# Optimization experiments

Measured on AMD Instinct MI355X. Metric: run time of the kernel, lower is better.

## Reference

```python
import math
import jax, jax.numpy as jnp
import numpy as np

B, L, H, D = 1, 2048, 16, 64
M = 24            # nb_features
WINDOW = 128      # local_context / window_size
SCALE = 0.125     # softmax_scale = 1/sqrt(D)
MASK_VAL = -10000.0
EPS = 1e-4        # SBPerformerFeatures eps


def setup_inputs() -> dict:
    key = jax.random.key(0)
    k1, k2 = jax.random.split(key)
    qkv = jax.random.normal(k1, (B, L, 3, H, D), dtype=jnp.float32)
    proj = jax.random.normal(k2, (M, D), dtype=jnp.float32)  # Performer random features
    return {"qkv": qkv, "proj": proj}


def _performer_features(x, proj, is_query):
    # Softmax-kernel random features with separate log scale (scatterbrain SBPerformerFeatures).
    # exp(t*q.k) ~= exp(q_log + k_log) * <q_prime, k_prime>
    dn = math.sqrt(SCALE)
    xs = x * dn                                            # (b,h,l,d)
    x_dash = jnp.einsum('bhld,md->bhlm', xs, proj)         # (b,h,l,m)
    x_norm = 0.5 * jnp.sum(xs * xs, axis=-1, keepdims=True)
    half_log_m = 0.5 * math.log(M)
    if is_query:
        stab = jax.lax.stop_gradient(jnp.max(x_dash, axis=-1, keepdims=True))
        prime = jnp.exp(x_dash - stab) + EPS               # per-row stabilized
        log_scale = stab - x_norm - half_log_m             # (b,h,l,1)
    else:
        stab = jax.lax.stop_gradient(jnp.max(x_dash, axis=(-1, -2), keepdims=True))
        prime = jnp.exp(x_dash - x_norm - stab) + EPS      # norm folded in (needed for cumsum)
        log_scale = stab - half_log_m                      # (b,h,1,1)
    return prime, log_scale


def _band_mask(n):
    idx = jnp.arange(n)
    diff = idx[:, None] - idx[None, :]                     # i - j
    return jnp.where((diff >= 0) & (diff <= WINDOW), 0.0, MASK_VAL)  # (L,L)


def _forward(qkv, proj):
    q, k, v = qkv[:, :, 0], qkv[:, :, 1], qkv[:, :, 2]     # (b,l,h,d)
    q = jnp.transpose(q, (0, 2, 1, 3))                     # (b,h,l,d)
    k = jnp.transpose(k, (0, 2, 1, 3))
    v = jnp.transpose(v, (0, 2, 1, 3))

    # --- GlobalPerformer path ---
    q_prime, q_log = _performer_features(q, proj, True)    # (b,h,l,m), (b,h,l,1)
    k_prime, k_log = _performer_features(k, proj, False)   # (b,h,l,m), (b,h,1,1)
    global_scale = q_log + k_log                           # (b,h,l,1)

    k_cum = jnp.cumsum(k_prime, axis=2)
    global_out_cumsum = jnp.einsum('bhlm,bhlm->bhl', q_prime, k_cum)
    # causal_dot_product: out_i = q'_i . sum_{j<=i} k'_j v_j^T
    kv = jnp.cumsum(k_prime[..., :, None] * v[..., None, :], axis=2)   # (b,h,l,m,d)
    global_out = jnp.einsum('bhlm,bhlmd->bhld', q_prime, kv)

    mask = _band_mask(L)
    p_scores = jnp.einsum('bhme,bhne->bhmn', q_prime, k_prime) * SCALE
    global_qk = jnp.maximum(p_scores + mask[None, None], 0.0)  # masked_fill(<=0, 0)

    # --- Local exact softmax path ---
    scores = jnp.einsum('bhme,bhne->bhmn', q, k) * SCALE
    local_qk = scores + mask[None, None]
    qk_lse = jax.scipy.special.logsumexp(local_qk, axis=-1, keepdims=True)  # (b,h,l,1)

    gqk_sum = jnp.sum(global_qk, axis=-1, keepdims=True)
    global_log_norm = jnp.log(jnp.maximum(global_out_cumsum[..., None] - gqk_sum, 1e-24)) + global_scale
    log_norm = jnp.logaddexp(qk_lse, global_log_norm)      # (b,h,l,1)
    global_prime_scale = jnp.exp(global_scale - log_norm)  # (b,h,l,1)

    local_score = jax.nn.softmax(local_qk - log_norm, axis=-1) - global_qk * global_prime_scale
    out = jnp.einsum('bhmn,bhnd->bhmd', local_score, v) + global_out * global_prime_scale
    return jnp.transpose(out, (0, 2, 1, 3))                # (b,l,h,d)


def reference(qkv, proj):
    return _forward(qkv, proj)
```

## Files before the change

kernel.cpp:

```cpp
#include <hip/hip_runtime.h>
#include <hip/hip_bf16.h>

#define L_SEQ 2048
#define NH 16
#define DH 64
#define NM 24
#define NCH 32
#define SCALE_F 0.125f
#define EPS_F 1e-4f
#define DN_F 0.35355339059327373f
#define HLM_F 1.5890269151739727f

typedef __attribute__((ext_vector_type(8))) short short8v;
typedef __attribute__((ext_vector_type(4))) float f32x4;

__device__ __forceinline__ unsigned short f2bf(float x) {
  unsigned u = __float_as_uint(x);
  u += 0x7FFFu + ((u >> 16) & 1u);
  return (unsigned short)(u >> 16);
}
__device__ __forceinline__ unsigned pk2(float a, float b) {
  return (unsigned)f2bf(a) | ((unsigned)f2bf(b) << 16);
}
__device__ __forceinline__ float stab_from_pmax(const float* __restrict__ pmax, int h, int t) {
  float v = pmax[h * 32 + (t & 31)];
  v = fmaxf(v, __shfl_xor(v, 1));  v = fmaxf(v, __shfl_xor(v, 2));
  v = fmaxf(v, __shfl_xor(v, 4));  v = fmaxf(v, __shfl_xor(v, 8));
  v = fmaxf(v, __shfl_xor(v, 16));
  return v;
}

__global__ __launch_bounds__(256) void k1_feat(
    const float* __restrict__ qkv, const float* __restrict__ proj,
    float* __restrict__ kdash, float* __restrict__ knorm,
    float* __restrict__ qdash, float* __restrict__ qnorm,
    float* __restrict__ pmax, unsigned* __restrict__ kbw, unsigned* __restrict__ qbw)
{
  __shared__ __attribute__((aligned(16))) float sP[24][68];
  __shared__ __attribute__((aligned(16))) float sX[64][68];
  __shared__ float sRed[256];
  const int c = blockIdx.x, h = blockIdx.y, t = threadIdx.x;
  for (int i = t; i < 24 * 64; i += 256) sP[i >> 6][i & 63] = proj[i];
  float lmax = -1e30f;
  const int r = t >> 2, mg = t & 3;
  for (int qk = 0; qk < 2; ++qk) {
    const int slot = qk ? 0 : 1;
    __syncthreads();
    for (int i = t; i < 1024; i += 256) {
      int rr = i >> 4, d4 = (i & 15) * 4;
      int l = c * 64 + rr;
      *(float4*)&sX[rr][d4] = *(const float4*)(qkv + (((size_t)l * 3 + slot) * NH + h) * DH + d4);
    }
    __syncthreads();
    unsigned* dstw = qk ? qbw : kbw;
    for (int w = t; w < 2048; w += 256) {
      int rr = w >> 5, wo = w & 31;
      int l = c * 64 + rr;
      float2 xv = *(const float2*)&sX[rr][2 * wo];
      dstw[((size_t)h * L_SEQ + l) * 32 + (wo ^ ((rr & 7) << 2))] = pk2(xv.x, xv.y);
    }
    float acc[6] = {0.f, 0.f, 0.f, 0.f, 0.f, 0.f};
    float sq = 0.f;
    for (int d4 = 0; d4 < 16; ++d4) {
      float4 xv = *(const float4*)&sX[r][d4 * 4];
      sq += xv.x * xv.x; sq += xv.y * xv.y; sq += xv.z * xv.z; sq += xv.w * xv.w;
#pragma unroll
      for (int i = 0; i < 6; ++i) {
        float4 pv = *(const float4*)&sP[mg * 6 + i][d4 * 4];
        acc[i] += xv.x * pv.x; acc[i] += xv.y * pv.y;
        acc[i] += xv.z * pv.z; acc[i] += xv.w * pv.w;
      }
    }
    int l = c * 64 + r;
    float* dsh = qk ? qdash : kdash;
#pragma unroll
    for (int i = 0; i < 6; ++i) {
      float v = acc[i] * DN_F;
      dsh[((size_t)h * L_SEQ + l) * 24 + mg * 6 + i] = v;
      if (!qk) lmax = fmaxf(lmax, v);
    }
    if (mg == 0) (qk ? qnorm : knorm)[h * L_SEQ + l] = 0.5f * SCALE_F * sq;
  }
  sRed[t] = lmax;
  __syncthreads();
#pragma unroll
  for (int s = 128; s > 0; s >>= 1) {
    if (t < s) sRed[t] = fmaxf(sRed[t], sRed[t + s]);
    __syncthreads();
  }
  if (t == 0) pmax[h * 32 + c] = sRed[0];
}

__global__ __launch_bounds__(256) void k3_kprime(
    const float* __restrict__ qkv, const float* __restrict__ kdash,
    const float* __restrict__ knorm, const float* __restrict__ pmax,
    unsigned* __restrict__ kpw, float* __restrict__ kpfx, float* __restrict__ kvs,
    unsigned* __restrict__ vtw)
{
  __shared__ float sKp[64][25];
  __shared__ __attribute__((aligned(16))) float sV[64][68];
  const int c = blockIdx.x, h = blockIdx.y, t = threadIdx.x;
  const float stab = stab_from_pmax(pmax, h, t);
  for (int i = t; i < 1024; i += 256) {
    int rr = i >> 4, d4 = (i & 15) * 4;
    int l = c * 64 + rr;
    *(float4*)&sV[rr][d4] = *(const float4*)(qkv + (((size_t)l * 3 + 2) * NH + h) * DH + d4);
  }
  for (int i = t; i < 1536; i += 256) {
    int r = i / 24, m = i % 24;
    int l = c * 64 + r;
    sKp[r][m] = __expf(kdash[((size_t)h * L_SEQ + l) * 24 + m] - knorm[h * L_SEQ + l] - stab) + EPS_F;
  }
  __syncthreads();
  for (int w = t; w < 1024; w += 256) {
    int r = w >> 4, wo = w & 15;
    int l = c * 64 + r;
    float a = (wo < 12) ? sKp[r][2 * wo] : 0.f;
    float bb = (wo < 12) ? sKp[r][2 * wo + 1] : 0.f;
    kpw[((size_t)h * L_SEQ + l) * 16 + (wo ^ ((r & 3) << 2))] = pk2(a, bb);
  }
  for (int w = t; w < 2048; w += 256) {
    int d = w >> 5, jp = w & 31;
    vtw[((size_t)h * NCH + c) * 2048 + d * 32 + (jp ^ ((d & 7) << 2))] = pk2(sV[2 * jp][d], sV[2 * jp + 1][d]);
  }
  if (t < 192) {
    const int m = t % 24, dO = (t / 24) * 8;
    float a0x = 0.f, a0y = 0.f, a0z = 0.f, a0w = 0.f;
    float a1x = 0.f, a1y = 0.f, a1z = 0.f, a1w = 0.f;
    for (int r2 = 0; r2 < 64; ++r2) {
      float kp = sKp[r2][m];
      float4 v0 = *(const float4*)&sV[r2][dO];
      float4 v1 = *(const float4*)&sV[r2][dO + 4];
      a0x += kp * v0.x; a0y += kp * v0.y; a0z += kp * v0.z; a0w += kp * v0.w;
      a1x += kp * v1.x; a1y += kp * v1.y; a1z += kp * v1.z; a1w += kp * v1.w;
    }
    float* dst = kvs + ((size_t)h * NCH + c) * 1536 + m * 64 + dO;
    float4 o0 = {a0x, a0y, a0z, a0w};
    float4 o1 = {a1x, a1y, a1z, a1w};
    *(float4*)dst = o0;
    *(float4*)(dst + 4) = o1;
  }
  if (t < 24) {
    float run = 0.f;
    for (int r2 = 0; r2 < 64; ++r2) {
      run += sKp[r2][t];
      kpfx[((size_t)h * L_SEQ + c * 64 + r2) * 24 + t] = run;
    }
  }
}

__global__ __launch_bounds__(256, 2) void k6_attn(
    const unsigned* __restrict__ kpw, const float* __restrict__ kpfx,
    const float* __restrict__ kvs, const unsigned* __restrict__ vtw,
    const float* __restrict__ qdash, const float* __restrict__ qnorm,
    const float* __restrict__ pmax, const unsigned* __restrict__ kbw,
    const unsigned* __restrict__ qbw, float* __restrict__ out)
{
  __shared__ __attribute__((aligned(16))) char lds[62304];
  char* sKW = lds;
  char* sKp = lds + 24576;
  char* sQV = lds + 36864;
  char* sQp = lds + 45056;
  float* sQpF = (float*)(lds + 49152);
  float* sSum = (float*)(lds + 55296);
  float* sGps = sSum + 64;
  float* sRin = sGps + 64;
  float* sKcx = (float*)(lds + 56064);
  float* sPfx = (float*)(lds + 56160);

  const int b = blockIdx.x, h = blockIdx.y, t = threadIdx.x;
  const int wv = t >> 6, lane = t & 63, g = lane >> 4, ln = lane & 15;
  const int keybase = b * 64 - 128;
  const int jmin = (b >= 2) ? 0 : (128 - 64 * b);
  const int rA = wv * 16 + ln;

  for (int w = t; w < 1536; w += 256) {
    int r = w >> 3, q4 = w & 7;
    int l = keybase + r; l = l < 0 ? 0 : l;
    *(uint4*)(sKW + r * 128 + q4 * 16) = *(const uint4*)(kbw + ((size_t)h * L_SEQ + l) * 32 + q4 * 4);
  }
  for (int w = t; w < 512; w += 256) {
    int r = w >> 3, q4 = w & 7;
    int l = b * 64 + r;
    *(uint4*)(sQV + r * 128 + q4 * 16) = *(const uint4*)(qbw + ((size_t)h * L_SEQ + l) * 32 + q4 * 4);
  }
  for (int w = t; w < 768; w += 256) {
    int r = w >> 2, q4 = w & 3;
    int l = keybase + r; l = l < 0 ? 0 : l;
    *(uint4*)(sKp + r * 64 + q4 * 16) = *(const uint4*)(kpw + ((size_t)h * L_SEQ + l) * 16 + q4 * 4);
  }
  const float stab = stab_from_pmax(pmax, h, t);
  {
    float accp[6] = {0.f, 0.f, 0.f, 0.f, 0.f, 0.f};
    for (int bp = 0; bp < b; ++bp) {
      const float* src = kvs + ((size_t)h * NCH + bp) * 1536;
#pragma unroll
      for (int j = 0; j < 6; ++j) accp[j] += src[t + j * 256];
    }
#pragma unroll
    for (int j = 0; j < 6; ++j) sPfx[t + j * 256] = accp[j];
  }
  if (t < 24) {
    float runk = 0.f;
    for (int bp = 0; bp < b; ++bp)
      runk += kpfx[((size_t)h * L_SEQ + bp * 64 + 63) * 24 + t];
    sKcx[t] = runk;
  }
  float qlog = 0.f;
  if (t < 64) {
    int r = t, l = b * 64 + r;
    const float* qdp = qdash + ((size_t)h * L_SEQ + l) * 24;
    float qd[24], mx = -1e30f;
#pragma unroll
    for (int m = 0; m < 24; ++m) { qd[m] = qdp[m]; mx = fmaxf(mx, qd[m]); }
    float qpv[24];
#pragma unroll
    for (int m = 0; m < 24; ++m) { qpv[m] = __expf(qd[m] - mx) + EPS_F; sQpF[r * 24 + m] = qpv[m]; }
    qlog = mx - qnorm[h * L_SEQ + l] - HLM_F;
#pragma unroll
    for (int wo = 0; wo < 16; ++wo) {
      float a = (wo < 12) ? qpv[2 * wo] : 0.f;
      float bb = (wo < 12) ? qpv[2 * wo + 1] : 0.f;
      *(unsigned*)(sQp + (r * 64 + (((wo * 4)) ^ ((r & 3) << 4)))) = pk2(a, bb);
    }
  }
  __syncthreads();

  float eF[12][4];
  float rs[4] = {0.f, 0.f, 0.f, 0.f};
  short8v aS0 = *(const short8v*)(sQV + (rA * 128 + ((g * 16) ^ ((rA & 7) << 4))));
  short8v aS1 = *(const short8v*)(sQV + (rA * 128 + ((64 + g * 16) ^ ((rA & 7) << 4))));
#pragma unroll
  for (int nt = 0; nt < 12; ++nt) {
    int rB = nt * 16 + ln;
    short8v b0 = *(const short8v*)(sKW + (rB * 128 + ((g * 16) ^ ((rB & 7) << 4))));
    short8v b1 = *(const short8v*)(sKW + (rB * 128 + ((64 + g * 16) ^ ((rB & 7) << 4))));
    f32x4 acc = {0.f, 0.f, 0.f, 0.f};
    acc = __builtin_amdgcn_mfma_f32_16x16x32_bf16(aS0, b0, acc, 0, 0, 0);
    acc = __builtin_amdgcn_mfma_f32_16x16x32_bf16(aS1, b1, acc, 0, 0, 0);
    int j = nt * 16 + ln;
#pragma unroll
    for (int reg = 0; reg < 4; ++reg) {
      int rl = wv * 16 + g * 4 + reg;
      float e = 0.f;
      if (j >= rl && j <= rl + 128 && j >= jmin) e = __expf(SCALE_F * acc[reg]);
      eF[nt][reg] = e;
      rs[reg] += e;
    }
  }
#pragma unroll
  for (int reg = 0; reg < 4; ++reg) {
    float v = rs[reg];
    v += __shfl_xor(v, 1); v += __shfl_xor(v, 2);
    v += __shfl_xor(v, 4); v += __shfl_xor(v, 8);
    if (ln == 0) sSum[wv * 16 + g * 4 + reg] = v;
  }

  float pF[12][4];
  short8v aP = *(const short8v*)(sQp + (rA * 64 + ((g * 16) ^ ((rA & 3) << 4))));
#pragma unroll
  for (int nt = 0; nt < 12; ++nt) {
    int rB = nt * 16 + ln;
    short8v bp = *(const short8v*)(sKp + (rB * 64 + ((g * 16) ^ ((rB & 3) << 4))));
    f32x4 acc = {0.f, 0.f, 0.f, 0.f};
    acc = __builtin_amdgcn_mfma_f32_16x16x32_bf16(aP, bp, acc, 0, 0, 0);
#pragma unroll
    for (int reg = 0; reg < 4; ++reg) pF[nt][reg] = acc[reg];
  }
  __syncthreads();

  if (t < 64) {
    int r = t, l = b * 64 + r;
    const float* kfc = kpfx + ((size_t)h * L_SEQ + l) * 24;
    int b1i = (b >= 1) ? b - 1 : 0;
    int b2i = (b >= 2) ? b - 2 : 0;
    int rm1 = (r >= 1) ? r - 1 : 0;
    const float* T1p = kpfx + ((size_t)h * L_SEQ + b1i * 64 + 63) * 24;
    const float* T2p = kpfx + ((size_t)h * L_SEQ + b2i * 64 + 63) * 24;
    const float* S2p = kpfx + ((size_t)h * L_SEQ + b2i * 64 + rm1) * 24;
    float f1 = (b >= 1) ? 1.f : 0.f;
    float f2 = (b >= 2) ? 1.f : 0.f;
    float fr = (b >= 2 && r >= 1) ? 1.f : 0.f;
    float psc = 0.f, kcs = 0.f, bnd = 0.f;
#pragma unroll
    for (int m = 0; m < 24; ++m) {
      float qp = sQpF[r * 24 + m];
      float kc = kfc[m];
      psc += qp * kc;
      kcs += qp * sKcx[m];
      bnd += qp * (kc + f1 * T1p[m] + f2 * T2p[m] - fr * S2p[m]);
    }
    float goc = kcs + psc;
    float gqk = SCALE_F * bnd;
    float se = sSum[r];
    float lse = __logf(se);
    float gscale = qlog + stab - HLM_F;
    float gln = __logf(fmaxf(goc - gqk, 1e-24f)) + gscale;
    float mx2 = fmaxf(lse, gln), mn2 = fminf(lse, gln);
    float lognorm = mx2 + log1pf(__expf(mn2 - mx2));
    sGps[r] = __expf(gscale - lognorm);
    sRin[r] = 1.f / se;
  }
  __syncthreads();

  float gpr[4], rin[4];
#pragma unroll
  for (int reg = 0; reg < 4; ++reg) {
    int rl = wv * 16 + g * 4 + reg;
    gpr[reg] = sGps[rl];
    rin[reg] = sRin[rl];
  }
#pragma unroll
  for (int nt = 0; nt < 12; ++nt) {
    int j = nt * 16 + ln;
#pragma unroll
    for (int reg = 0; reg < 4; ++reg) {
      int rl = wv * 16 + g * 4 + reg;
      bool causal = (j >= 128) && (j <= 128 + rl);
      bool bprev = (j >= rl) && (j < 128) && (j >= jmin);
      float coef = causal ? (1.f - SCALE_F) * gpr[reg] : (bprev ? -SCALE_F * gpr[reg] : 0.f);
      float wgt = eF[nt][reg] * rin[reg] + coef * pF[nt][reg];
      float wn = __shfl_xor(wgt, 1);
      if ((ln & 1) == 0) {
        *(unsigned*)(sKW + (rl * 384 + ((j * 2) ^ ((rl & 7) << 4)))) = pk2(wgt, wn);
      }
    }
  }
  __syncthreads();

  for (int w = t; w < 1024; w += 256) {
    int d = w >> 4, mp = w & 15;
    int m0 = 2 * mp, m1 = m0 + 1;
    float a = (m0 < 24) ? sPfx[m0 * 64 + d] : 0.f;
    float bb = (m1 < 24) ? sPfx[m1 * 64 + d] : 0.f;
    *(unsigned*)(sKp + (d * 64 + ((mp * 4) ^ ((d & 3) << 4)))) = pk2(a, bb);
  }

  f32x4 oF[4];
#pragma unroll
  for (int dt = 0; dt < 4; ++dt) { f32x4 z = {0.f, 0.f, 0.f, 0.f}; oF[dt] = z; }
  for (int vt3 = 0; vt3 < 3; ++vt3) {
    int lt = b - 2 + vt3; lt = lt < 0 ? 0 : lt;
    for (int w = t; w < 512; w += 256) {
      *(uint4*)(sQV + w * 16) = *(const uint4*)(vtw + ((size_t)h * NCH + lt) * 2048 + w * 4);
    }
    __syncthreads();
#pragma unroll
    for (int ks = 0; ks < 2; ++ks) {
      short8v aw = *(const short8v*)(sKW + (rA * 384 + ((vt3 * 128 + ks * 64 + g * 16) ^ ((rA & 7) << 4))));
#pragma unroll
      for (int dt = 0; dt < 4; ++dt) {
        int rB = dt * 16 + ln;
        short8v bv = *(const short8v*)(sQV + (rB * 128 + ((ks * 64 + g * 16) ^ ((rB & 7) << 4))));
        oF[dt] = __builtin_amdgcn_mfma_f32_16x16x32_bf16(aw, bv, oF[dt], 0, 0, 0);
      }
    }
    __syncthreads();
  }

  short8v aq = *(const short8v*)(sQp + (rA * 64 + ((g * 16) ^ ((rA & 3) << 4))));
  f32x4 ogF[4];
#pragma unroll
  for (int dt = 0; dt < 4; ++dt) {
    int rB = dt * 16 + ln;
    short8v bg = *(const short8v*)(sKp + (rB * 64 + ((g * 16) ^ ((rB & 3) << 4))));
    f32x4 z = {0.f, 0.f, 0.f, 0.f};
    ogF[dt] = __builtin_amdgcn_mfma_f32_16x16x32_bf16(aq, bg, z, 0, 0, 0);
  }

#pragma unroll
  for (int dt = 0; dt < 4; ++dt) {
    int d = dt * 16 + ln;
#pragma unroll
    for (int reg = 0; reg < 4; ++reg) {
      int rl = wv * 16 + g * 4 + reg;
      int l = b * 64 + rl;
      out[((size_t)l * NH + h) * DH + d] = oF[dt][reg] + gpr[reg] * ogF[dt][reg];
    }
  }
}

extern "C" void kernel_launch(void* const* d_in, const int* in_sizes, int n_in,
                              void* d_out, int out_size, void* d_ws, size_t ws_size,
                              hipStream_t stream)
{
  const float* qkv = (const float*)d_in[0];
  const float* proj = (const float*)d_in[1];
  float* out = (float*)d_out;
  char* ws = (char*)d_ws;

  float* kdash   = (float*)(ws + 0);
  float* qdash   = (float*)(ws + 3145728);
  float* knorm   = (float*)(ws + 6291456);
  float* qnorm   = (float*)(ws + 6422528);
  float* pmax    = (float*)(ws + 6553600);
  unsigned* kbw  = (unsigned*)(ws + 6555648);
  unsigned* qbw  = (unsigned*)(ws + 10749952);
  unsigned* kpw  = (unsigned*)(ws + 14944256);
  float* kpfx    = (float*)(ws + 17041408);
  unsigned* vtw  = (unsigned*)(ws + 20187136);
  float* kvs     = (float*)(ws + 24381440);

  k1_feat<<<dim3(32, 16), 256, 0, stream>>>(qkv, proj, kdash, knorm, qdash, qnorm, pmax, kbw, qbw);
  k3_kprime<<<dim3(32, 16), 256, 0, stream>>>(qkv, kdash, knorm, pmax, kpw, kpfx, kvs, vtw);
  k6_attn<<<dim3(32, 16), 256, 0, stream>>>(kpw, kpfx, kvs, vtw, qdash, qnorm, pmax, kbw, qbw, out);
}
```

Measured before the change: 125.7 us.

## Fuse three attention kernels into one cooperative kernel with grid syncs

Replaces the three-kernel pipeline (feature projection, key-prime/prefix, attention) with one cooperative kernel that uses two grid-wide syncs. Query features, bf16 tiles and V tiles stay in LDS across phases, so the qdash/qnorm/qbw workspace round trips and two launch gaps go away. The prefix-sum loop over kvs chunks is also unrolled by four to raise memory-level parallelism. The cost is grid.sync overhead and the constraint that all 512 blocks must be co-resident, which is why the launch asks for two blocks per CU and roughly 80KB of LDS each. If the cooperative launch fails, it falls back to the original three kernels.

```diff
diff --git a/kernel.cpp b/kernel.cpp
--- a/kernel.cpp
+++ b/kernel.cpp
@@ -1,10 +1,12 @@
 #include <hip/hip_runtime.h>
 #include <hip/hip_bf16.h>
+#include <hip/hip_cooperative_groups.h>
+
+namespace cg = cooperative_groups;
 
 #define L_SEQ 2048
 #define NH 16
 #define DH 64
-#define NM 24
 #define NCH 32
 #define SCALE_F 0.125f
 #define EPS_F 1e-4f
@@ -28,6 +30,396 @@
   v = fmaxf(v, __shfl_xor(v, 4));  v = fmaxf(v, __shfl_xor(v, 8));
   v = fmaxf(v, __shfl_xor(v, 16));
   return v;
+}
+
+#define LDS_BYTES 80512
+
+__global__ __launch_bounds__(256, 2) void fused_attn(
+    const float* __restrict__ qkv, const float* __restrict__ proj,
+    float* __restrict__ pmax, unsigned* __restrict__ kbw,
+    unsigned* __restrict__ kpw, float* __restrict__ kpfx,
+    float* __restrict__ kvs, unsigned* __restrict__ vtw,
+    float* __restrict__ out)
+{
+  __shared__ __align__(16) char lds[LDS_BYTES];
+  char* A  = lds;
+  char* B  = lds + 24576;
+  char* C  = lds + 36864;
+  char* D  = lds + 45056;
+  char* E  = lds + 53248;
+  char* F  = lds + 61440;
+  float* G = (float*)(lds + 65536);
+  float* H = (float*)(lds + 71680);
+  float* sRed  = (float*)(lds + 78336);
+  float* qlogA = (float*)(lds + 79360);
+  float* sKcx  = (float*)(lds + 79616);
+  float* sSum  = (float*)(lds + 79744);
+  float* sGps  = (float*)(lds + 80000);
+  float* sRin  = (float*)(lds + 80256);
+
+  const int b = blockIdx.x, h = blockIdx.y, t = threadIdx.x;
+  const int r4 = t >> 2, mg = t & 3;
+  cg::grid_group grid = cg::this_grid();
+
+  float* sP = (float*)D;
+  float* sX = (float*)A;
+  for (int i = t; i < 1536; i += 256) sP[(i >> 6) * 68 + (i & 63)] = proj[i];
+
+  float kd[6];
+  float sqk = 0.f;
+  float lmax = -1e30f;
+
+  for (int qk = 0; qk < 2; ++qk) {
+    const int slot = qk ? 0 : 1;
+    __syncthreads();
+    for (int i = t; i < 1024; i += 256) {
+      int rr = i >> 4, q = i & 15;
+      int l = b * 64 + rr;
+      *(float4*)&sX[rr * 64 + 4 * (q ^ (rr & 15))] =
+          *(const float4*)(qkv + (((size_t)l * 3 + slot) * NH + h) * DH + 4 * q);
+    }
+    __syncthreads();
+    for (int w = t; w < 2048; w += 256) {
+      int rr = w >> 5, wo = w & 31;
+      int q = wo >> 1, sub = (wo & 1) * 2;
+      const float* px = &sX[rr * 64 + 4 * (q ^ (rr & 15)) + sub];
+      unsigned word = pk2(px[0], px[1]);
+      int swo = wo ^ ((rr & 7) << 2);
+      if (qk == 0) {
+        kbw[((size_t)h * L_SEQ + b * 64 + rr) * 32 + swo] = word;
+        *(unsigned*)(A + 16384 + rr * 128 + 4 * swo) = word;
+      } else {
+        *(unsigned*)(C + rr * 128 + 4 * swo) = word;
+      }
+    }
+    float acc[6] = {0.f, 0.f, 0.f, 0.f, 0.f, 0.f};
+    float sq = 0.f;
+    for (int d4 = 0; d4 < 16; ++d4) {
+      float4 xv = *(const float4*)&sX[r4 * 64 + 4 * (d4 ^ (r4 & 15))];
+      sq += xv.x * xv.x; sq += xv.y * xv.y; sq += xv.z * xv.z; sq += xv.w * xv.w;
+#pragma unroll
+      for (int i = 0; i < 6; ++i) {
+        float4 pv = *(const float4*)&sP[(mg * 6 + i) * 68 + d4 * 4];
+        acc[i] += xv.x * pv.x; acc[i] += xv.y * pv.y;
+        acc[i] += xv.z * pv.z; acc[i] += xv.w * pv.w;
+      }
+    }
+    if (qk == 0) {
+#pragma unroll
+      for (int i = 0; i < 6; ++i) { kd[i] = acc[i] * DN_F; lmax = fmaxf(lmax, kd[i]); }
+      sqk = sq;
+    } else {
+      float qd6[6]; float mx = -1e30f;
+#pragma unroll
+      for (int i = 0; i < 6; ++i) { qd6[i] = acc[i] * DN_F; mx = fmaxf(mx, qd6[i]); }
+      mx = fmaxf(mx, __shfl_xor(mx, 1));
+      mx = fmaxf(mx, __shfl_xor(mx, 2));
+      float qpv[6];
+#pragma unroll
+      for (int i = 0; i < 6; ++i) {
+        qpv[i] = __expf(qd6[i] - mx) + EPS_F;
+        G[r4 * 24 + mg * 6 + i] = qpv[i];
+      }
+#pragma unroll
+      for (int j = 0; j < 3; ++j)
+        *(unsigned*)(F + r4 * 64 + 4 * ((3 * mg + j) ^ ((r4 & 3) << 2))) = pk2(qpv[2 * j], qpv[2 * j + 1]);
+      if (mg == 0) {
+#pragma unroll
+        for (int j = 0; j < 4; ++j)
+          *(unsigned*)(F + r4 * 64 + 4 * ((12 + j) ^ ((r4 & 3) << 2))) = 0u;
+        qlogA[r4] = mx - 0.5f * SCALE_F * sq - HLM_F;
+      }
+    }
+  }
+  sRed[t] = lmax;
+  __syncthreads();
+#pragma unroll
+  for (int s = 128; s > 0; s >>= 1) {
+    if (t < s) sRed[t] = fmaxf(sRed[t], sRed[t + s]);
+    __syncthreads();
+  }
+  if (t == 0) pmax[h * 32 + b] = sRed[0];
+
+  grid.sync();
+
+  const float stab = stab_from_pmax(pmax, h, t);
+  float* sV = (float*)A;
+  for (int i = t; i < 1024; i += 256) {
+    int rr = i >> 4, q = i & 15;
+    int l = b * 64 + rr;
+    *(float4*)&sV[rr * 64 + 4 * (q ^ (rr & 15))] =
+        *(const float4*)(qkv + (((size_t)l * 3 + 2) * NH + h) * DH + 4 * q);
+  }
+  float* sKpF = H;
+  {
+    float kn = 0.5f * SCALE_F * sqk;
+    float kp6[6];
+#pragma unroll
+    for (int i = 0; i < 6; ++i) {
+      kp6[i] = __expf(kd[i] - kn - stab) + EPS_F;
+      sKpF[r4 * 25 + mg * 6 + i] = kp6[i];
+    }
+#pragma unroll
+    for (int j = 0; j < 3; ++j) {
+      unsigned word = pk2(kp6[2 * j], kp6[2 * j + 1]);
+      int swo = (3 * mg + j) ^ ((r4 & 3) << 2);
+      kpw[((size_t)h * L_SEQ + b * 64 + r4) * 16 + swo] = word;
+      *(unsigned*)(B + 8192 + r4 * 64 + 4 * swo) = word;
+    }
+    if (mg == 0) {
+#pragma unroll
+      for (int j = 0; j < 4; ++j) {
+        int swo = (12 + j) ^ ((r4 & 3) << 2);
+        kpw[((size_t)h * L_SEQ + b * 64 + r4) * 16 + swo] = 0u;
+        *(unsigned*)(B + 8192 + r4 * 64 + 4 * swo) = 0u;
+      }
+    }
+  }
+  __syncthreads();
+  for (int w = t; w < 2048; w += 256) {
+    int d = w >> 5, jp = w & 31;
+    int ra = 2 * jp, rb = 2 * jp + 1, q = d >> 2, s4 = d & 3;
+    float va = sV[ra * 64 + 4 * (q ^ (ra & 15)) + s4];
+    float vb = sV[rb * 64 + 4 * (q ^ (rb & 15)) + s4];
+    unsigned word = pk2(va, vb);
+    int swo = jp ^ ((d & 7) << 2);
+    vtw[((size_t)h * NCH + b) * 2048 + d * 32 + swo] = word;
+    *(unsigned*)(E + d * 128 + 4 * swo) = word;
+  }
+  if (t < 192) {
+    const int m = t % 24, dO = (t / 24) * 8;
+    const int s0 = dO >> 2, s1 = s0 + 1;
+    float a0x = 0.f, a0y = 0.f, a0z = 0.f, a0w = 0.f;
+    float a1x = 0.f, a1y = 0.f, a1z = 0.f, a1w = 0.f;
+    for (int r2 = 0; r2 < 64; ++r2) {
+      float kp = sKpF[r2 * 25 + m];
+      float4 v0 = *(const float4*)&sV[r2 * 64 + 4 * (s0 ^ (r2 & 15))];
+      float4 v1 = *(const float4*)&sV[r2 * 64 + 4 * (s1 ^ (r2 & 15))];
+      a0x += kp * v0.x; a0y += kp * v0.y; a0z += kp * v0.z; a0w += kp * v0.w;
+      a1x += kp * v1.x; a1y += kp * v1.y; a1z += kp * v1.z; a1w += kp * v1.w;
+    }
+    float* dst = kvs + ((size_t)h * NCH + b) * 1536 + m * 64 + dO;
+    float4 o0 = {a0x, a0y, a0z, a0w};
+    float4 o1 = {a1x, a1y, a1z, a1w};
+    *(float4*)dst = o0;
+    *(float4*)(dst + 4) = o1;
+  }
+  if (t < 24) {
+    float run = 0.f;
+    for (int r2 = 0; r2 < 64; ++r2) {
+      run += sKpF[r2 * 25 + t];
+      kpfx[((size_t)h * L_SEQ + b * 64 + r2) * 24 + t] = run;
+    }
+  }
+
+  grid.sync();
+
+  const int wv = t >> 6, lane = t & 63, g = lane >> 4, ln = lane & 15;
+  const int keybase = b * 64 - 128;
+  const int jmin = (b >= 2) ? 0 : (128 - 64 * b);
+  const int rA = wv * 16 + ln;
+
+  for (int w = t; w < 1024; w += 256) {
+    int r = w >> 3, q4 = w & 7;
+    int l = keybase + r; l = l < 0 ? 0 : l;
+    *(uint4*)(A + r * 128 + q4 * 16) = *(const uint4*)(kbw + ((size_t)h * L_SEQ + l) * 32 + q4 * 4);
+  }
+  for (int w = t; w < 512; w += 256) {
+    int r = w >> 2, q4 = w & 3;
+    int l = keybase + r; l = l < 0 ? 0 : l;
+    *(uint4*)(B + r * 64 + q4 * 16) = *(const uint4*)(kpw + ((size_t)h * L_SEQ + l) * 16 + q4 * 4);
+  }
+  {
+    float accp[6] = {0.f, 0.f, 0.f, 0.f, 0.f, 0.f};
+    const float* srcb = kvs + (size_t)h * NCH * 1536 + t;
+    int bp = 0;
+    for (; bp + 4 <= b; bp += 4) {
+      float v0[6], v1[6], v2[6], v3[6];
+#pragma unroll
+      for (int j = 0; j < 6; ++j) v0[j] = srcb[(size_t)(bp + 0) * 1536 + j * 256];
+#pragma unroll
+      for (int j = 0; j < 6; ++j) v1[j] = srcb[(size_t)(bp + 1) * 1536 + j * 256];
+#pragma unroll
+      for (int j = 0; j < 6; ++j) v2[j] = srcb[(size_t)(bp + 2) * 1536 + j * 256];
+#pragma unroll
+      for (int j = 0; j < 6; ++j) v3[j] = srcb[(size_t)(bp + 3) * 1536 + j * 256];
+#pragma unroll
+      for (int j = 0; j < 6; ++j) {
+        accp[j] += v0[j]; accp[j] += v1[j]; accp[j] += v2[j]; accp[j] += v3[j];
+      }
+    }
+    for (; bp < b; ++bp) {
+#pragma unroll
+      for (int j = 0; j < 6; ++j) accp[j] += srcb[(size_t)bp * 1536 + j * 256];
+    }
+#pragma unroll
+    for (int j = 0; j < 6; ++j) H[t + j * 256] = accp[j];
+  }
+  if (t < 24) {
+    float runk = 0.f;
+    for (int bp = 0; bp < b; ++bp)
+      runk += kpfx[((size_t)h * L_SEQ + bp * 64 + 63) * 24 + t];
+    sKcx[t] = runk;
+  }
+  __syncthreads();
+
+  float eF[12][4];
+  float rs[4] = {0.f, 0.f, 0.f, 0.f};
+  short8v aS0 = *(const short8v*)(C + (rA * 128 + ((g * 16) ^ ((rA & 7) << 4))));
+  short8v aS1 = *(const short8v*)(C + (rA * 128 + ((64 + g * 16) ^ ((rA & 7) << 4))));
+#pragma unroll
+  for (int nt = 0; nt < 12; ++nt) {
+    int rB = nt * 16 + ln;
+    short8v b0 = *(const short8v*)(A + (rB * 128 + ((g * 16) ^ ((rB & 7) << 4))));
+    short8v b1 = *(const short8v*)(A + (rB * 128 + ((64 + g * 16) ^ ((rB & 7) << 4))));
+    f32x4 acc = {0.f, 0.f, 0.f, 0.f};
+    acc = __builtin_amdgcn_mfma_f32_16x16x32_bf16(aS0, b0, acc, 0, 0, 0);
+    acc = __builtin_amdgcn_mfma_f32_16x16x32_bf16(aS1, b1, acc, 0, 0, 0);
+    int j = nt * 16 + ln;
+#pragma unroll
+    for (int reg = 0; reg < 4; ++reg) {
+      int rl = wv * 16 + g * 4 + reg;
+      float e = 0.f;
+      if (j >= rl && j <= rl + 128 && j >= jmin) e = __expf(SCALE_F * acc[reg]);
+      eF[nt][reg] = e;
+      rs[reg] += e;
+    }
+  }
+#pragma unroll
+  for (int reg = 0; reg < 4; ++reg) {
+    float v = rs[reg];
+    v += __shfl_xor(v, 1); v += __shfl_xor(v, 2);
+    v += __shfl_xor(v, 4); v += __shfl_xor(v, 8);
+    if (ln == 0) sSum[wv * 16 + g * 4 + reg] = v;
+  }
+
+  float pF[12][4];
+  short8v aP = *(const short8v*)(F + (rA * 64 + ((g * 16) ^ ((rA & 3) << 4))));
+#pragma unroll
+  for (int nt = 0; nt < 12; ++nt) {
+    int rB = nt * 16 + ln;
+    short8v bp = *(const short8v*)(B + (rB * 64 + ((g * 16) ^ ((rB & 3) << 4))));
+    f32x4 acc = {0.f, 0.f, 0.f, 0.f};
+    acc = __builtin_amdgcn_mfma_f32_16x16x32_bf16(aP, bp, acc, 0, 0, 0);
+#pragma unroll
+    for (int reg = 0; reg < 4; ++reg) pF[nt][reg] = acc[reg];
+  }
+  __syncthreads();
+
+  if (t < 64) {
+    int r = t, l = b * 64 + r;
+    const float* kfc = kpfx + ((size_t)h * L_SEQ + l) * 24;
+    int b1i = (b >= 1) ? b - 1 : 0;
+    int b2i = (b >= 2) ? b - 2 : 0;
+    int rm1 = (r >= 1) ? r - 1 : 0;
+    const float* T1p = kpfx + ((size_t)h * L_SEQ + b1i * 64 + 63) * 24;
+    const float* T2p = kpfx + ((size_t)h * L_SEQ + b2i * 64 + 63) * 24;
+    const float* S2p = kpfx + ((size_t)h * L_SEQ + b2i * 64 + rm1) * 24;
+    float f1 = (b >= 1) ? 1.f : 0.f;
+    float f2 = (b >= 2) ? 1.f : 0.f;
+    float fr = (b >= 2 && r >= 1) ? 1.f : 0.f;
+    float psc = 0.f, kcs = 0.f, bnd = 0.f;
+#pragma unroll
+    for (int m = 0; m < 24; ++m) {
+      float qp = G[r * 24 + m];
+      float kc = kfc[m];
+      psc += qp * kc;
+      kcs += qp * sKcx[m];
+      bnd += qp * (kc + f1 * T1p[m] + f2 * T2p[m] - fr * S2p[m]);
+    }
+    float goc = kcs + psc;
+    float gqk = SCALE_F * bnd;
+    float se = sSum[r];
+    float lse = __logf(se);
+    float gscale = qlogA[r] + stab - HLM_F;
+    float gln = __logf(fmaxf(goc - gqk, 1e-24f)) + gscale;
+    float mx2 = fmaxf(lse, gln), mn2 = fminf(lse, gln);
+    float lognorm = mx2 + log1pf(__expf(mn2 - mx2));
+    sGps[r] = __expf(gscale - lognorm);
+    sRin[r] = 1.f / se;
+  }
+  __syncthreads();
+
+  float gpr[4], rin[4];
+#pragma unroll
+  for (int reg = 0; reg < 4; ++reg) {
+    int rl = wv * 16 + g * 4 + reg;
+    gpr[reg] = sGps[rl];
+    rin[reg] = sRin[rl];
+  }
+#pragma unroll
+  for (int nt = 0; nt < 12; ++nt) {
+    int j = nt * 16 + ln;
+#pragma unroll
+    for (int reg = 0; reg < 4; ++reg) {
+      int rl = wv * 16 + g * 4 + reg;
+      bool causal = (j >= 128) && (j <= 128 + rl);
+      bool bprev = (j >= rl) && (j < 128) && (j >= jmin);
+      float coef = causal ? (1.f - SCALE_F) * gpr[reg] : (bprev ? -SCALE_F * gpr[reg] : 0.f);
+      float wgt = eF[nt][reg] * rin[reg] + coef * pF[nt][reg];
+      float wn = __shfl_xor(wgt, 1);
+      if ((ln & 1) == 0) {
+        *(unsigned*)(A + (rl * 384 + ((j * 2) ^ ((rl & 7) << 4)))) = pk2(wgt, wn);
+      }
+    }
+  }
+  __syncthreads();
+
+  for (int w = t; w < 1024; w += 256) {
+    int d = w >> 4, mp = w & 15;
+    int m0 = 2 * mp, m1 = m0 + 1;
+    float a = (m0 < 24) ? H[m0 * 64 + d] : 0.f;
+    float bb = (m1 < 24) ? H[m1 * 64 + d] : 0.f;
+    *(unsigned*)(B + (d * 64 + ((mp * 4) ^ ((d & 3) << 4)))) = pk2(a, bb);
+  }
+
+  f32x4 oF[4];
+#pragma unroll
+  for (int dt = 0; dt < 4; ++dt) { f32x4 z = {0.f, 0.f, 0.f, 0.f}; oF[dt] = z; }
+  for (int vt3 = 0; vt3 < 3; ++vt3) {
+    const char* vbase;
+    if (vt3 < 2) {
+      int lt = b - 2 + vt3; lt = lt < 0 ? 0 : lt;
+      for (int w = t; w < 512; w += 256)
+        *(uint4*)(D + w * 16) = *(const uint4*)(vtw + ((size_t)h * NCH + lt) * 2048 + w * 4);
+      vbase = D;
+    } else {
+      vbase = E;
+    }
+    __syncthreads();
+#pragma unroll
+    for (int ks = 0; ks < 2; ++ks) {
+      short8v aw = *(const short8v*)(A + (rA * 384 + ((vt3 * 128 + ks * 64 + g * 16) ^ ((rA & 7) << 4))));
+#pragma unroll
+      for (int dt = 0; dt < 4; ++dt) {
+        int rB = dt * 16 + ln;
+        short8v bv = *(const short8v*)(vbase + (rB * 128 + ((ks * 64 + g * 16) ^ ((rB & 7) << 4))));
+        oF[dt] = __builtin_amdgcn_mfma_f32_16x16x32_bf16(aw, bv, oF[dt], 0, 0, 0);
+      }
+    }
+    __syncthreads();
+  }
+
+  short8v aq = *(const short8v*)(F + (rA * 64 + ((g * 16) ^ ((rA & 3) << 4))));
+  f32x4 ogF[4];
+#pragma unroll
+  for (int dt = 0; dt < 4; ++dt) {
+    int rB = dt * 16 + ln;
+    short8v bg = *(const short8v*)(B + (rB * 64 + ((g * 16) ^ ((rB & 3) << 4))));
+    f32x4 z = {0.f, 0.f, 0.f, 0.f};
+    ogF[dt] = __builtin_amdgcn_mfma_f32_16x16x32_bf16(aq, bg, z, 0, 0, 0);
+  }
+
+#pragma unroll
+  for (int dt = 0; dt < 4; ++dt) {
+    int d = dt * 16 + ln;
+#pragma unroll
+    for (int reg = 0; reg < 4; ++reg) {
+      int rl = wv * 16 + g * 4 + reg;
+      int l = b * 64 + rl;
+      out[((size_t)l * NH + h) * DH + d] = oF[dt][reg] + gpr[reg] * ogF[dt][reg];
+    }
+  }
 }
 
 __global__ __launch_bounds__(256) void k1_feat(
@@ -192,10 +584,26 @@
   const float stab = stab_from_pmax(pmax, h, t);
   {
     float accp[6] = {0.f, 0.f, 0.f, 0.f, 0.f, 0.f};
-    for (int bp = 0; bp < b; ++bp) {
-      const float* src = kvs + ((size_t)h * NCH + bp) * 1536;
-#pragma unroll
-      for (int j = 0; j < 6; ++j) accp[j] += src[t + j * 256];
+    const float* srcb = kvs + (size_t)h * NCH * 1536 + t;
+    int bp = 0;
+    for (; bp + 4 <= b; bp += 4) {
+      float v0[6], v1[6], v2[6], v3[6];
+#pragma unroll
+      for (int j = 0; j < 6; ++j) v0[j] = srcb[(size_t)(bp + 0) * 1536 + j * 256];
+#pragma unroll
+      for (int j = 0; j < 6; ++j) v1[j] = srcb[(size_t)(bp + 1) * 1536 + j * 256];
+#pragma unroll
+      for (int j = 0; j < 6; ++j) v2[j] = srcb[(size_t)(bp + 2) * 1536 + j * 256];
+#pragma unroll
+      for (int j = 0; j < 6; ++j) v3[j] = srcb[(size_t)(bp + 3) * 1536 + j * 256];
+#pragma unroll
+      for (int j = 0; j < 6; ++j) {
+        accp[j] += v0[j]; accp[j] += v1[j]; accp[j] += v2[j]; accp[j] += v3[j];
+      }
+    }
+    for (; bp < b; ++bp) {
+#pragma unroll
+      for (int j = 0; j < 6; ++j) accp[j] += srcb[(size_t)bp * 1536 + j * 256];
     }
 #pragma unroll
     for (int j = 0; j < 6; ++j) sPfx[t + j * 256] = accp[j];
@@ -389,19 +797,26 @@
   float* out = (float*)d_out;
   char* ws = (char*)d_ws;
 
-  float* kdash   = (float*)(ws + 0);
-  float* qdash   = (float*)(ws + 3145728);
-  float* knorm   = (float*)(ws + 6291456);
-  float* qnorm   = (float*)(ws + 6422528);
-  float* pmax    = (float*)(ws + 6553600);
-  unsigned* kbw  = (unsigned*)(ws + 6555648);
-  unsigned* qbw  = (unsigned*)(ws + 10749952);
-  unsigned* kpw  = (unsigned*)(ws + 14944256);
-  float* kpfx    = (float*)(ws + 17041408);
-  unsigned* vtw  = (unsigned*)(ws + 20187136);
-  float* kvs     = (float*)(ws + 24381440);
-
-  k1_feat<<<dim3(32, 16), 256, 0, stream>>>(qkv, proj, kdash, knorm, qdash, qnorm, pmax, kbw, qbw);
-  k3_kprime<<<dim3(32, 16), 256, 0, stream>>>(qkv, kdash, knorm, pmax, kpw, kpfx, kvs, vtw);
-  k6_attn<<<dim3(32, 16), 256, 0, stream>>>(kpw, kpfx, kvs, vtw, qdash, qnorm, pmax, kbw, qbw, out);
+  float* pmax    = (float*)(ws + 0);
+  unsigned* kbw  = (unsigned*)(ws + 4096);
+  unsigned* kpw  = (unsigned*)(ws + 4198400);
+  float* kpfx    = (float*)(ws + 6295552);
+  float* kvs     = (float*)(ws + 9441280);
+  unsigned* vtw  = (unsigned*)(ws + 12587008);
+  float* kdash   = (float*)(ws + 16781312);
+  float* qdash   = (float*)(ws + 19927040);
+  float* knorm   = (float*)(ws + 23072768);
+  float* qnorm   = (float*)(ws + 23203840);
+  unsigned* qbw  = (unsigned*)(ws + 23334912);
+
+  void* args[] = {
+      (void*)&qkv, (void*)&proj, (void*)&pmax, (void*)&kbw, (void*)&kpw,
+      (void*)&kpfx, (void*)&kvs, (void*)&vtw, (void*)&out};
+  hipError_t err = hipLaunchCooperativeKernel((const void*)fused_attn, dim3(NCH, NH, 1),
+                                              dim3(256, 1, 1), args, 0, stream);
+  if (err != hipSuccess) {
+    k1_feat<<<dim3(NCH, NH), 256, 0, stream>>>(qkv, proj, kdash, knorm, qdash, qnorm, pmax, kbw, qbw);
+    k3_kprime<<<dim3(NCH, NH), 256, 0, stream>>>(qkv, kdash, knorm, pmax, kpw, kpfx, kvs, vtw);
+    k6_attn<<<dim3(NCH, NH), 256, 0, stream>>>(kpw, kpfx, kvs, vtw, qdash, qnorm, pmax, kbw, qbw, out);
+  }
 }
```

Result: slower. 215.6 us (+71.4%).

## Split q/k feature work across grid z, unroll kvs prefix loads, keep q-prime in registers

Applied to the files above, without the earlier changes.

The feature kernel now launches a third grid dimension so the query and key halves run in separate blocks instead of a serial loop, doubling the block count to 1024. In the attention kernel, the prefix sum over per-chunk kv states issues four chunks' loads before accumulating, exposing more memory-level parallelism. The q-prime values stay in registers instead of a shared-memory staging array, which shrinks LDS use. This may raise register pressure in the attention kernel, which is already launch-bounded to 2 blocks per SM.

```diff
diff --git a/kernel.cpp b/kernel.cpp
--- a/kernel.cpp
+++ b/kernel.cpp
@@ -4,7 +4,6 @@
 #define L_SEQ 2048
 #define NH 16
 #define DH 64
-#define NM 24
 #define NCH 32
 #define SCALE_F 0.125f
 #define EPS_F 1e-4f
@@ -39,56 +38,55 @@
   __shared__ __attribute__((aligned(16))) float sP[24][68];
   __shared__ __attribute__((aligned(16))) float sX[64][68];
   __shared__ float sRed[256];
-  const int c = blockIdx.x, h = blockIdx.y, t = threadIdx.x;
+  const int c = blockIdx.x, h = blockIdx.y, qk = blockIdx.z, t = threadIdx.x;
+  const int slot = qk ? 0 : 1;
   for (int i = t; i < 24 * 64; i += 256) sP[i >> 6][i & 63] = proj[i];
+  for (int i = t; i < 1024; i += 256) {
+    int rr = i >> 4, d4 = (i & 15) * 4;
+    int l = c * 64 + rr;
+    *(float4*)&sX[rr][d4] = *(const float4*)(qkv + (((size_t)l * 3 + slot) * NH + h) * DH + d4);
+  }
+  __syncthreads();
+  unsigned* dstw = qk ? qbw : kbw;
+  for (int w = t; w < 2048; w += 256) {
+    int rr = w >> 5, wo = w & 31;
+    int l = c * 64 + rr;
+    float2 xv = *(const float2*)&sX[rr][2 * wo];
+    dstw[((size_t)h * L_SEQ + l) * 32 + (wo ^ ((rr & 7) << 2))] = pk2(xv.x, xv.y);
+  }
+  const int r = t >> 2, mg = t & 3;
+  float acc[6] = {0.f, 0.f, 0.f, 0.f, 0.f, 0.f};
+  float sq = 0.f;
+  for (int d4 = 0; d4 < 16; ++d4) {
+    float4 xv = *(const float4*)&sX[r][d4 * 4];
+    sq += xv.x * xv.x; sq += xv.y * xv.y; sq += xv.z * xv.z; sq += xv.w * xv.w;
+#pragma unroll
+    for (int i = 0; i < 6; ++i) {
+      float4 pv = *(const float4*)&sP[mg * 6 + i][d4 * 4];
+      acc[i] += xv.x * pv.x; acc[i] += xv.y * pv.y;
+      acc[i] += xv.z * pv.z; acc[i] += xv.w * pv.w;
+    }
+  }
+  int l = c * 64 + r;
+  float* dsh = qk ? qdash : kdash;
   float lmax = -1e30f;
-  const int r = t >> 2, mg = t & 3;
-  for (int qk = 0; qk < 2; ++qk) {
-    const int slot = qk ? 0 : 1;
+#pragma unroll
+  for (int i = 0; i < 6; ++i) {
+    float v = acc[i] * DN_F;
+    dsh[((size_t)h * L_SEQ + l) * 24 + mg * 6 + i] = v;
+    lmax = fmaxf(lmax, v);
+  }
+  if (mg == 0) (qk ? qnorm : knorm)[h * L_SEQ + l] = 0.5f * SCALE_F * sq;
+  if (qk == 0) {
+    sRed[t] = lmax;
     __syncthreads();
-    for (int i = t; i < 1024; i += 256) {
-      int rr = i >> 4, d4 = (i & 15) * 4;
-      int l = c * 64 + rr;
-      *(float4*)&sX[rr][d4] = *(const float4*)(qkv + (((size_t)l * 3 + slot) * NH + h) * DH + d4);
-    }
-    __syncthreads();
-    unsigned* dstw = qk ? qbw : kbw;
-    for (int w = t; w < 2048; w += 256) {
-      int rr = w >> 5, wo = w & 31;
-      int l = c * 64 + rr;
-      float2 xv = *(const float2*)&sX[rr][2 * wo];
-      dstw[((size_t)h * L_SEQ + l) * 32 + (wo ^ ((rr & 7) << 2))] = pk2(xv.x, xv.y);
-    }
-    float acc[6] = {0.f, 0.f, 0.f, 0.f, 0.f, 0.f};
-    float sq = 0.f;
-    for (int d4 = 0; d4 < 16; ++d4) {
-      float4 xv = *(const float4*)&sX[r][d4 * 4];
-      sq += xv.x * xv.x; sq += xv.y * xv.y; sq += xv.z * xv.z; sq += xv.w * xv.w;
-#pragma unroll
-      for (int i = 0; i < 6; ++i) {
-        float4 pv = *(const float4*)&sP[mg * 6 + i][d4 * 4];
-        acc[i] += xv.x * pv.x; acc[i] += xv.y * pv.y;
-        acc[i] += xv.z * pv.z; acc[i] += xv.w * pv.w;
-      }
-    }
-    int l = c * 64 + r;
-    float* dsh = qk ? qdash : kdash;
-#pragma unroll
-    for (int i = 0; i < 6; ++i) {
-      float v = acc[i] * DN_F;
-      dsh[((size_t)h * L_SEQ + l) * 24 + mg * 6 + i] = v;
-      if (!qk) lmax = fmaxf(lmax, v);
-    }
-    if (mg == 0) (qk ? qnorm : knorm)[h * L_SEQ + l] = 0.5f * SCALE_F * sq;
-  }
-  sRed[t] = lmax;
-  __syncthreads();
-#pragma unroll
-  for (int s = 128; s > 0; s >>= 1) {
-    if (t < s) sRed[t] = fmaxf(sRed[t], sRed[t + s]);
-    __syncthreads();
-  }
-  if (t == 0) pmax[h * 32 + c] = sRed[0];
+#pragma unroll
+    for (int s = 128; s > 0; s >>= 1) {
+      if (t < s) sRed[t] = fmaxf(sRed[t], sRed[t + s]);
+      __syncthreads();
+    }
+    if (t == 0) pmax[h * 32 + c] = sRed[0];
+  }
 }
 
 __global__ __launch_bounds__(256) void k3_kprime(
@@ -156,17 +154,16 @@
     const float* __restrict__ pmax, const unsigned* __restrict__ kbw,
     const unsigned* __restrict__ qbw, float* __restrict__ out)
 {
-  __shared__ __attribute__((aligned(16))) char lds[62304];
+  __shared__ __attribute__((aligned(16))) char lds[56160];
   char* sKW = lds;
   char* sKp = lds + 24576;
   char* sQV = lds + 36864;
   char* sQp = lds + 45056;
-  float* sQpF = (float*)(lds + 49152);
-  float* sSum = (float*)(lds + 55296);
+  float* sSum = (float*)(lds + 49152);
   float* sGps = sSum + 64;
   float* sRin = sGps + 64;
-  float* sKcx = (float*)(lds + 56064);
-  float* sPfx = (float*)(lds + 56160);
+  float* sKcx = (float*)(lds + 49920);
+  float* sPfx = (float*)(lds + 50016);
 
   const int b = blockIdx.x, h = blockIdx.y, t = threadIdx.x;
   const int wv = t >> 6, lane = t & 63, g = lane >> 4, ln = lane & 15;
@@ -192,10 +189,26 @@
   const float stab = stab_from_pmax(pmax, h, t);
   {
     float accp[6] = {0.f, 0.f, 0.f, 0.f, 0.f, 0.f};
-    for (int bp = 0; bp < b; ++bp) {
-      const float* src = kvs + ((size_t)h * NCH + bp) * 1536;
-#pragma unroll
-      for (int j = 0; j < 6; ++j) accp[j] += src[t + j * 256];
+    const float* srcb = kvs + (size_t)h * NCH * 1536 + t;
+    int bp = 0;
+    for (; bp + 4 <= b; bp += 4) {
+      float v0[6], v1[6], v2[6], v3[6];
+#pragma unroll
+      for (int j = 0; j < 6; ++j) v0[j] = srcb[(size_t)(bp + 0) * 1536 + j * 256];
+#pragma unroll
+      for (int j = 0; j < 6; ++j) v1[j] = srcb[(size_t)(bp + 1) * 1536 + j * 256];
+#pragma unroll
+      for (int j = 0; j < 6; ++j) v2[j] = srcb[(size_t)(bp + 2) * 1536 + j * 256];
+#pragma unroll
+      for (int j = 0; j < 6; ++j) v3[j] = srcb[(size_t)(bp + 3) * 1536 + j * 256];
+#pragma unroll
+      for (int j = 0; j < 6; ++j) {
+        accp[j] += v0[j]; accp[j] += v1[j]; accp[j] += v2[j]; accp[j] += v3[j];
+      }
+    }
+    for (; bp < b; ++bp) {
+#pragma unroll
+      for (int j = 0; j < 6; ++j) accp[j] += srcb[(size_t)bp * 1536 + j * 256];
     }
 #pragma unroll
     for (int j = 0; j < 6; ++j) sPfx[t + j * 256] = accp[j];
@@ -207,15 +220,15 @@
     sKcx[t] = runk;
   }
   float qlog = 0.f;
+  float qpv[24];
   if (t < 64) {
     int r = t, l = b * 64 + r;
     const float* qdp = qdash + ((size_t)h * L_SEQ + l) * 24;
     float qd[24], mx = -1e30f;
 #pragma unroll
     for (int m = 0; m < 24; ++m) { qd[m] = qdp[m]; mx = fmaxf(mx, qd[m]); }
-    float qpv[24];
-#pragma unroll
-    for (int m = 0; m < 24; ++m) { qpv[m] = __expf(qd[m] - mx) + EPS_F; sQpF[r * 24 + m] = qpv[m]; }
+#pragma unroll
+    for (int m = 0; m < 24; ++m) qpv[m] = __expf(qd[m] - mx) + EPS_F;
     qlog = mx - qnorm[h * L_SEQ + l] - HLM_F;
 #pragma unroll
     for (int wo = 0; wo < 16; ++wo) {
@@ -284,7 +297,7 @@
     float psc = 0.f, kcs = 0.f, bnd = 0.f;
 #pragma unroll
     for (int m = 0; m < 24; ++m) {
-      float qp = sQpF[r * 24 + m];
+      float qp = qpv[m];
       float kc = kfc[m];
       psc += qp * kc;
       kcs += qp * sKcx[m];
@@ -401,7 +414,7 @@
   unsigned* vtw  = (unsigned*)(ws + 20187136);
   float* kvs     = (float*)(ws + 24381440);
 
-  k1_feat<<<dim3(32, 16), 256, 0, stream>>>(qkv, proj, kdash, knorm, qdash, qnorm, pmax, kbw, qbw);
-  k3_kprime<<<dim3(32, 16), 256, 0, stream>>>(qkv, kdash, knorm, pmax, kpw, kpfx, kvs, vtw);
-  k6_attn<<<dim3(32, 16), 256, 0, stream>>>(kpw, kpfx, kvs, vtw, qdash, qnorm, pmax, kbw, qbw, out);
-}
+  k1_feat<<<dim3(NCH, NH, 2), 256, 0, stream>>>(qkv, proj, kdash, knorm, qdash, qnorm, pmax, kbw, qbw);
+  k3_kprime<<<dim3(NCH, NH), 256, 0, stream>>>(qkv, kdash, knorm, pmax, kpw, kpfx, kvs, vtw);
+  k6_attn<<<dim3(NCH, NH), 256, 0, stream>>>(kpw, kpfx, kvs, vtw, qdash, qnorm, pmax, kbw, qbw, out);
+}
```

New measurement: 120.6 us. 1.04x faster.
